# Performance work log

Hardware: AMD Instinct MI355X
Metric: run time of the kernel (lower is better)

## Reference

```python
import jax, jax.numpy as jnp
import numpy as np

B, S, D, H = 2, 2048, 1024, 16
HD = D // H

def setup_inputs() -> dict:
    key = jax.random.key(0)
    ks = jax.random.split(key, 7)
    s = 1.0 / np.sqrt(D)
    return {
        "x": jax.random.normal(ks[0], (B, S, D), dtype=jnp.float32),
        "Wq": jax.random.uniform(ks[1], (D, D), jnp.float32, -s, s),
        "bq": jax.random.uniform(ks[2], (D,), jnp.float32, -s, s),
        "Wk": jax.random.uniform(ks[3], (D, D), jnp.float32, -s, s),
        "bk": jax.random.uniform(ks[4], (D,), jnp.float32, -s, s),
        "Wv": jax.random.uniform(ks[5], (D, D), jnp.float32, -s, s),
        "bv": jax.random.uniform(ks[6], (D,), jnp.float32, -s, s),
    }

def reference(x, Wq, bq, Wk, bk, Wv, bv):
    b, s, d = x.shape
    def proj(W, bias):
        # [b,s,d] -> [b,H,s,hd]
        y = x @ W + bias
        return y.reshape(b, s, H, HD).transpose(0, 2, 1, 3)
    Q = proj(Wq, bq)
    K = proj(Wk, bk)
    V = proj(Wv, bv)
    # NOTE: original scales by head_dim**0.5 (not sqrt) -> divide by sqrt(HD)
    scores = jnp.einsum("bhqd,bhkd->bhqk", Q, K) / (HD ** 0.5)
    attn = jax.nn.softmax(scores, axis=-1)
    out = jnp.einsum("bhqk,bhkd->bhqd", attn, V)
    out = out.transpose(0, 2, 1, 3).reshape(b, s, d)
    return out + x
```

## Files before the change

kernel.cpp:

```cpp
#include <hip/hip_runtime.h>
#include <stdint.h>

typedef float f32x4 __attribute__((ext_vector_type(4)));
typedef __bf16 bf16x8 __attribute__((ext_vector_type(8)));

union Frag {
    bf16x8 v;
    uint32_t u[4];
    __bf16 e[8];
    uint4 q;
};

constexpr int B_ = 2, S_ = 2048, D_ = 1024, H_ = 16, HD_ = 64;
constexpr int M_ = B_ * S_;

__host__ __device__ constexpr int kperm(int kl) {
    return ((kl & 12) << 1) | ((kl & 16) >> 2) | (kl & 3);
}

typedef const __attribute__((address_space(1))) char gch_t;
typedef __attribute__((address_space(3))) char lch_t;
#define GLD(g, l) __builtin_amdgcn_global_load_lds((gch_t*)(g), (lch_t*)(l), 16, 0, 0)

#define MFMA16(a, b, c) __builtin_amdgcn_mfma_f32_16x16x32_bf16((a), (b), (c), 0, 0, 0)

__global__ void k_cast_x(const float* __restrict__ x, __bf16* __restrict__ xb) {
    int t = blockIdx.x * 256 + threadIdx.x;
    const float4* src = (const float4*)(x + (size_t)t * 32);
    __bf16 buf[32];
#pragma unroll
    for (int j = 0; j < 8; ++j) {
        float4 f = src[j];
        buf[kperm(4 * j + 0)] = (__bf16)f.x;
        buf[kperm(4 * j + 1)] = (__bf16)f.y;
        buf[kperm(4 * j + 2)] = (__bf16)f.z;
        buf[kperm(4 * j + 3)] = (__bf16)f.w;
    }
    uint4* dst = (uint4*)(xb + (size_t)t * 32);
#pragma unroll
    for (int j = 0; j < 4; ++j) dst[j] = ((const uint4*)buf)[j];
}

__global__ void k_prep_w(const float* __restrict__ Wq, const float* __restrict__ Wk,
                         const float* __restrict__ Wv, __bf16* __restrict__ Wt) {
    __shared__ float tile[32][33];
    int p = blockIdx.z;
    const float* W = (p == 0) ? Wq : (p == 1 ? Wk : Wv);
    int n0 = blockIdx.x * 32, k0 = blockIdx.y * 32;
    int tx = threadIdx.x, ty = threadIdx.y;
#pragma unroll
    for (int t = 0; t < 4; ++t)
        tile[ty + 8 * t][tx] = W[(size_t)(k0 + ty + 8 * t) * D_ + n0 + tx];
    __syncthreads();
#pragma unroll
    for (int t = 0; t < 4; ++t)
        Wt[(size_t)(p * D_ + n0 + ty + 8 * t) * D_ + k0 + kperm(tx)] = (__bf16)tile[tx][ty + 8 * t];
}

__global__ __launch_bounds__(256) void k_qkv(
        const __bf16* __restrict__ xb, const __bf16* __restrict__ Wt,
        const float* __restrict__ bq, const float* __restrict__ bk, const float* __restrict__ bv,
        __bf16* __restrict__ Qb, __bf16* __restrict__ Kb, __bf16* __restrict__ Vt) {
    __shared__ __align__(16) char ldsA[128 * 128];
    __shared__ __align__(16) char ldsB[128 * 128];

    const int tid = threadIdx.x;
    const int m0 = blockIdx.x * 128, n0 = blockIdx.y * 128;
    const int lane = tid & 63, w = tid >> 6;
    const int wr = w >> 1, wc = w & 1;
    const int g = lane >> 4, qr = lane & 15, qr7 = qr & 7;
    const int lr = lane >> 3, lp = lane & 7;
    const int c = lp ^ lr;

    const __bf16* aSrc = xb + (size_t)(m0 + w * 32 + lr) * D_ + c * 8;
    const __bf16* bSrc = Wt + (size_t)(n0 + w * 32 + lr) * D_ + c * 8;
    char* aDst = ldsA + (w * 32) * 128;
    char* bDst = ldsB + (w * 32) * 128;

    f32x4 acc[4][4] = {};

    for (int kk = 0; kk < D_; kk += 64) {
#pragma unroll
        for (int j = 0; j < 4; ++j) {
            GLD(aSrc + kk + j * (8 * D_), aDst + j * (8 * 128));
            GLD(bSrc + kk + j * (8 * D_), bDst + j * (8 * 128));
        }
        __syncthreads();

#pragma unroll
        for (int kc = 0; kc < 2; ++kc) {
            Frag afr[4], bfr[4];
#pragma unroll
            for (int mi = 0; mi < 4; ++mi) {
                int r = wr * 64 + mi * 16 + qr;
                afr[mi].q = *(const uint4*)(ldsA + r * 128 + (((4 * kc + g) ^ qr7) << 4));
            }
#pragma unroll
            for (int ni = 0; ni < 4; ++ni) {
                int r = wc * 64 + ni * 16 + qr;
                bfr[ni].q = *(const uint4*)(ldsB + r * 128 + (((4 * kc + g) ^ qr7) << 4));
            }
#pragma unroll
            for (int mi = 0; mi < 4; ++mi)
#pragma unroll
                for (int ni = 0; ni < 4; ++ni)
                    acc[mi][ni] = MFMA16(afr[mi].v, bfr[ni].v, acc[mi][ni]);
        }
        __syncthreads();
    }

    const int p = n0 >> 10;
    const float* bias = (p == 0) ? bq : (p == 1 ? bk : bv);
#pragma unroll
    for (int ni = 0; ni < 4; ++ni) {
        int n = n0 + wc * 64 + ni * 16 + qr;
        int d = n & 1023;
        float bb = bias[d];
        int h = d >> 6, hd = d & 63;
        int hd_s = (hd & 32) | kperm(hd & 31);
#pragma unroll
        for (int mi = 0; mi < 4; ++mi) {
#pragma unroll
            for (int r = 0; r < 4; ++r) {
                int m = m0 + wr * 64 + mi * 16 + 4 * g + r;
                float vv = acc[mi][ni][r] + bb;
                int b = m >> 11, s = m & 2047;
                if (p == 0) {
                    vv *= 0.125f;
                    Qb[((size_t)((b * H_ + h) * S_ + s)) * HD_ + hd_s] = (__bf16)vv;
                } else if (p == 1) {
                    Kb[((size_t)((b * H_ + h) * S_ + s)) * HD_ + hd_s] = (__bf16)vv;
                } else {
                    int s_s = (s & ~31) | kperm(s & 31);
                    Vt[((size_t)((b * H_ + h) * HD_ + hd)) * S_ + s_s] = (__bf16)vv;
                }
            }
        }
    }
}

__global__ __launch_bounds__(256) void k_attn(
        const __bf16* __restrict__ Qb, const __bf16* __restrict__ Kb,
        const __bf16* __restrict__ Vt, const float* __restrict__ x,
        float* __restrict__ out) {
    __shared__ __align__(16) char ldsK[64 * 128];
    __shared__ __align__(16) char ldsV[64 * 128];

    const int tid = threadIdx.x;
    const int q0 = blockIdx.x * 64;
    const int bh = blockIdx.y;
    const int lane = tid & 63, w = tid >> 6;
    const int g = lane >> 4, qr = lane & 15, qr7 = qr & 7;
    const int lr = lane >> 3, lp = lane & 7;
    const int c = lp ^ lr;
    const int qrow = q0 + w * 16 + qr;

    Frag qf[2];
    const __bf16* qp = Qb + ((size_t)bh * S_ + qrow) * HD_;
    qf[0].q = *(const uint4*)(qp + g * 8);
    qf[1].q = *(const uint4*)(qp + 32 + g * 8);

    const __bf16* kSrc = Kb + ((size_t)bh * S_ + w * 16 + lr) * HD_ + c * 8;
    const __bf16* vSrc = Vt + ((size_t)bh * HD_ + w * 16 + lr) * S_ + c * 8;
    char* kDst = ldsK + (w * 16) * 128;
    char* vDst = ldsV + (w * 16) * 128;

    f32x4 oacc[4] = {};
    f32x4 lacc = {};
    float mrun = -INFINITY;
    const float L2E = 1.44269504f;
    const float THR = 5.545177f;

    Frag ones;
    ones.u[0] = ones.u[1] = ones.u[2] = ones.u[3] = 0x3f803f80u;

    for (int kv0 = 0; kv0 < S_; kv0 += 64) {
        GLD(kSrc + (size_t)kv0 * HD_,            kDst);
        GLD(kSrc + (size_t)kv0 * HD_ + 8 * HD_,  kDst + 8 * 128);
        GLD(vSrc + kv0,                          vDst);
        GLD(vSrc + kv0 + 8 * S_,                 vDst + 8 * 128);
        __syncthreads();

        f32x4 sc[4];
#pragma unroll
        for (int kt = 0; kt < 4; ++kt) {
            const char* base = ldsK + (kt * 16 + qr) * 128;
            Frag k0, k1;
            k0.q = *(const uint4*)(base + ((g ^ qr7) << 4));
            k1.q = *(const uint4*)(base + (((4 + g) ^ qr7) << 4));
            f32x4 z = {};
            z = MFMA16(k0.v, qf[0].v, z);
            z = MFMA16(k1.v, qf[1].v, z);
            sc[kt] = z;
        }

        float tmax = -INFINITY;
#pragma unroll
        for (int kt = 0; kt < 4; ++kt)
#pragma unroll
            for (int r = 0; r < 4; ++r) tmax = fmaxf(tmax, sc[kt][r]);
        tmax = fmaxf(tmax, __shfl_xor(tmax, 16, 64));
        tmax = fmaxf(tmax, __shfl_xor(tmax, 32, 64));

        if (__any(tmax > mrun + THR)) {
            float mnew = fmaxf(mrun, tmax);
            float scale = __builtin_amdgcn_exp2f((mrun - mnew) * L2E);
            mrun = mnew;
            float scr[4];
#pragma unroll
            for (int r = 0; r < 4; ++r) scr[r] = __shfl(scale, (lane & 48) | (4 * g + r), 64);
#pragma unroll
            for (int ni = 0; ni < 4; ++ni)
#pragma unroll
                for (int r = 0; r < 4; ++r) oacc[ni][r] *= scr[r];
#pragma unroll
            for (int r = 0; r < 4; ++r) lacc[r] *= scr[r];
        }

        float m2 = mrun * L2E;
        Frag pa[2];
#pragma unroll
        for (int r = 0; r < 4; ++r) {
            pa[0].e[r]     = (__bf16)__builtin_amdgcn_exp2f(fmaf(sc[0][r], L2E, -m2));
            pa[0].e[4 + r] = (__bf16)__builtin_amdgcn_exp2f(fmaf(sc[1][r], L2E, -m2));
            pa[1].e[r]     = (__bf16)__builtin_amdgcn_exp2f(fmaf(sc[2][r], L2E, -m2));
            pa[1].e[4 + r] = (__bf16)__builtin_amdgcn_exp2f(fmaf(sc[3][r], L2E, -m2));
        }

        lacc = MFMA16(pa[0].v, ones.v, lacc);
        lacc = MFMA16(pa[1].v, ones.v, lacc);

#pragma unroll
        for (int ni = 0; ni < 4; ++ni) {
            const char* base = ldsV + (ni * 16 + qr) * 128;
            Frag v0, v1;
            v0.q = *(const uint4*)(base + ((g ^ qr7) << 4));
            v1.q = *(const uint4*)(base + (((4 + g) ^ qr7) << 4));
            oacc[ni] = MFMA16(pa[0].v, v0.v, oacc[ni]);
            oacc[ni] = MFMA16(pa[1].v, v1.v, oacc[ni]);
        }
        __syncthreads();
    }

    float rs[4];
#pragma unroll
    for (int r = 0; r < 4; ++r) rs[r] = 1.0f / lacc[r];

    int b = bh >> 4, h = bh & 15;
#pragma unroll
    for (int ni = 0; ni < 4; ++ni) {
#pragma unroll
        for (int r = 0; r < 4; ++r) {
            int q = q0 + w * 16 + 4 * g + r;
            size_t addr = ((size_t)(b * S_ + q)) * D_ + h * 64 + ni * 16 + qr;
            out[addr] = oacc[ni][r] * rs[r] + x[addr];
        }
    }
}

extern "C" void kernel_launch(void* const* d_in, const int* in_sizes, int n_in,
                              void* d_out, int out_size, void* d_ws, size_t ws_size,
                              hipStream_t stream) {
    const float* x  = (const float*)d_in[0];
    const float* Wq = (const float*)d_in[1];
    const float* bq = (const float*)d_in[2];
    const float* Wk = (const float*)d_in[3];
    const float* bk = (const float*)d_in[4];
    const float* Wv = (const float*)d_in[5];
    const float* bv = (const float*)d_in[6];
    float* out = (float*)d_out;

    char* ws = (char*)d_ws;
    __bf16* xb = (__bf16*)(ws);
    __bf16* Wt = (__bf16*)(ws + 8388608);
    __bf16* Qb = (__bf16*)(ws + 14680064);
    __bf16* Kb = (__bf16*)(ws + 23068672);
    __bf16* Vt = (__bf16*)(ws + 31457280);

    k_cast_x<<<512, 256, 0, stream>>>(x, xb);
    k_prep_w<<<dim3(32, 32, 3), dim3(32, 8), 0, stream>>>(Wq, Wk, Wv, Wt);
    k_qkv<<<dim3(32, 24), 256, 0, stream>>>(xb, Wt, bq, bk, bv, Qb, Kb, Vt);
    k_attn<<<dim3(32, 32), 256, 0, stream>>>(Qb, Kb, Vt, x, out);
}
```

Before: 119.2 us.

## Double-buffer LDS tiles in QKV GEMM and attention to overlap loads with MFMA

```diff
diff --git a/kernel.cpp b/kernel.cpp
--- a/kernel.cpp
+++ b/kernel.cpp
@@ -61,8 +61,8 @@
         const __bf16* __restrict__ xb, const __bf16* __restrict__ Wt,
         const float* __restrict__ bq, const float* __restrict__ bk, const float* __restrict__ bv,
         __bf16* __restrict__ Qb, __bf16* __restrict__ Kb, __bf16* __restrict__ Vt) {
-    __shared__ __align__(16) char ldsA[128 * 128];
-    __shared__ __align__(16) char ldsB[128 * 128];
+    __shared__ __align__(16) char ldsA[2][128 * 128];
+    __shared__ __align__(16) char ldsB[2][128 * 128];
 
     const int tid = threadIdx.x;
     const int m0 = blockIdx.x * 128, n0 = blockIdx.y * 128;
@@ -74,31 +74,30 @@
 
     const __bf16* aSrc = xb + (size_t)(m0 + w * 32 + lr) * D_ + c * 8;
     const __bf16* bSrc = Wt + (size_t)(n0 + w * 32 + lr) * D_ + c * 8;
-    char* aDst = ldsA + (w * 32) * 128;
-    char* bDst = ldsB + (w * 32) * 128;
+    const int dstOff = (w * 32) * 128;
 
     f32x4 acc[4][4] = {};
 
-    for (int kk = 0; kk < D_; kk += 64) {
+    auto STAGE = [&](int buf, int kk) {
 #pragma unroll
         for (int j = 0; j < 4; ++j) {
-            GLD(aSrc + kk + j * (8 * D_), aDst + j * (8 * 128));
-            GLD(bSrc + kk + j * (8 * D_), bDst + j * (8 * 128));
-        }
-        __syncthreads();
-
+            GLD(aSrc + kk + j * (8 * D_), ldsA[buf] + dstOff + j * (8 * 128));
+            GLD(bSrc + kk + j * (8 * D_), ldsB[buf] + dstOff + j * (8 * 128));
+        }
+    };
+    auto COMPUTE = [&](int buf) {
 #pragma unroll
         for (int kc = 0; kc < 2; ++kc) {
             Frag afr[4], bfr[4];
 #pragma unroll
             for (int mi = 0; mi < 4; ++mi) {
                 int r = wr * 64 + mi * 16 + qr;
-                afr[mi].q = *(const uint4*)(ldsA + r * 128 + (((4 * kc + g) ^ qr7) << 4));
+                afr[mi].q = *(const uint4*)(ldsA[buf] + r * 128 + (((4 * kc + g) ^ qr7) << 4));
             }
 #pragma unroll
             for (int ni = 0; ni < 4; ++ni) {
                 int r = wc * 64 + ni * 16 + qr;
-                bfr[ni].q = *(const uint4*)(ldsB + r * 128 + (((4 * kc + g) ^ qr7) << 4));
+                bfr[ni].q = *(const uint4*)(ldsB[buf] + r * 128 + (((4 * kc + g) ^ qr7) << 4));
             }
 #pragma unroll
             for (int mi = 0; mi < 4; ++mi)
@@ -106,8 +105,22 @@
                 for (int ni = 0; ni < 4; ++ni)
                     acc[mi][ni] = MFMA16(afr[mi].v, bfr[ni].v, acc[mi][ni]);
         }
+    };
+
+    STAGE(0, 0);
+    __syncthreads();
+    for (int t = 0; t < 14; t += 2) {
+        STAGE(1, (t + 1) * 64);
+        COMPUTE(0);
         __syncthreads();
-    }
+        STAGE(0, (t + 2) * 64);
+        COMPUTE(1);
+        __syncthreads();
+    }
+    STAGE(1, 15 * 64);
+    COMPUTE(0);
+    __syncthreads();
+    COMPUTE(1);
 
     const int p = n0 >> 10;
     const float* bias = (p == 0) ? bq : (p == 1 ? bk : bv);
@@ -143,8 +156,8 @@
         const __bf16* __restrict__ Qb, const __bf16* __restrict__ Kb,
         const __bf16* __restrict__ Vt, const float* __restrict__ x,
         float* __restrict__ out) {
-    __shared__ __align__(16) char ldsK[64 * 128];
-    __shared__ __align__(16) char ldsV[64 * 128];
+    __shared__ __align__(16) char ldsK[2][64 * 128];
+    __shared__ __align__(16) char ldsV[2][64 * 128];
 
     const int tid = threadIdx.x;
     const int q0 = blockIdx.x * 64;
@@ -162,8 +175,7 @@
 
     const __bf16* kSrc = Kb + ((size_t)bh * S_ + w * 16 + lr) * HD_ + c * 8;
     const __bf16* vSrc = Vt + ((size_t)bh * HD_ + w * 16 + lr) * S_ + c * 8;
-    char* kDst = ldsK + (w * 16) * 128;
-    char* vDst = ldsV + (w * 16) * 128;
+    const int dstOff = (w * 16) * 128;
 
     f32x4 oacc[4] = {};
     f32x4 lacc = {};
@@ -174,17 +186,19 @@
     Frag ones;
     ones.u[0] = ones.u[1] = ones.u[2] = ones.u[3] = 0x3f803f80u;
 
-    for (int kv0 = 0; kv0 < S_; kv0 += 64) {
-        GLD(kSrc + (size_t)kv0 * HD_,            kDst);
-        GLD(kSrc + (size_t)kv0 * HD_ + 8 * HD_,  kDst + 8 * 128);
-        GLD(vSrc + kv0,                          vDst);
-        GLD(vSrc + kv0 + 8 * S_,                 vDst + 8 * 128);
-        __syncthreads();
-
+    auto STAGE = [&](int buf, int kv0) {
+        GLD(kSrc + (size_t)kv0 * HD_,           ldsK[buf] + dstOff);
+        GLD(kSrc + (size_t)kv0 * HD_ + 8 * HD_, ldsK[buf] + dstOff + 8 * 128);
+        GLD(vSrc + kv0,                         ldsV[buf] + dstOff);
+        GLD(vSrc + kv0 + 8 * S_,                ldsV[buf] + dstOff + 8 * 128);
+    };
+
+    auto TILE = [&](int buf) {
         f32x4 sc[4];
+        __builtin_amdgcn_s_setprio(1);
 #pragma unroll
         for (int kt = 0; kt < 4; ++kt) {
-            const char* base = ldsK + (kt * 16 + qr) * 128;
+            const char* base = ldsK[buf] + (kt * 16 + qr) * 128;
             Frag k0, k1;
             k0.q = *(const uint4*)(base + ((g ^ qr7) << 4));
             k1.q = *(const uint4*)(base + (((4 + g) ^ qr7) << 4));
@@ -193,6 +207,7 @@
             z = MFMA16(k1.v, qf[1].v, z);
             sc[kt] = z;
         }
+        __builtin_amdgcn_s_setprio(0);
 
         float tmax = -INFINITY;
 #pragma unroll
@@ -227,20 +242,36 @@
             pa[1].e[4 + r] = (__bf16)__builtin_amdgcn_exp2f(fmaf(sc[3][r], L2E, -m2));
         }
 
+        __builtin_amdgcn_s_setprio(1);
         lacc = MFMA16(pa[0].v, ones.v, lacc);
         lacc = MFMA16(pa[1].v, ones.v, lacc);
 
 #pragma unroll
         for (int ni = 0; ni < 4; ++ni) {
-            const char* base = ldsV + (ni * 16 + qr) * 128;
+            const char* base = ldsV[buf] + (ni * 16 + qr) * 128;
             Frag v0, v1;
             v0.q = *(const uint4*)(base + ((g ^ qr7) << 4));
             v1.q = *(const uint4*)(base + (((4 + g) ^ qr7) << 4));
             oacc[ni] = MFMA16(pa[0].v, v0.v, oacc[ni]);
             oacc[ni] = MFMA16(pa[1].v, v1.v, oacc[ni]);
         }
+        __builtin_amdgcn_s_setprio(0);
+    };
+
+    STAGE(0, 0);
+    __syncthreads();
+    for (int t = 0; t < 30; t += 2) {
+        STAGE(1, (t + 1) * 64);
+        TILE(0);
         __syncthreads();
-    }
+        STAGE(0, (t + 2) * 64);
+        TILE(1);
+        __syncthreads();
+    }
+    STAGE(1, 31 * 64);
+    TILE(0);
+    __syncthreads();
+    TILE(1);
 
     float rs[4];
 #pragma unroll
```

Result: no change. 118.0 us (-1.0%).
